# Optimization experiments

Hardware: AMD Instinct MI355X
Metric: run time of the kernel (lower is better)

The kernel has to match this reference:

```python
import jax, jax.numpy as jnp
import numpy as np
from jax import lax

HEADS = 8
DIM_HEAD = 64
DIM = 512
EPS = 1e-12  # torch F.normalize eps


def _l2norm(x):
    # normalize along last axis, torch-style: x / max(||x||, eps)
    n = jnp.sqrt(jnp.sum(x * x, axis=-1, keepdims=True))
    return x / jnp.maximum(n, EPS)


def _dwconv(x_nchw, w):
    # depthwise 3x3, stride 1, SAME padding, no bias
    return lax.conv_general_dilated(
        x_nchw, w, window_strides=(1, 1), padding='SAME',
        dimension_numbers=('NCHW', 'OIHW', 'NCHW'),
        feature_group_count=DIM)


def setup_inputs() -> dict:
    key = jax.random.key(0)
    ks = jax.random.split(key, 8)
    b, h, w, c = 4, 128, 128, DIM
    s = 1.0 / np.sqrt(c)
    return {
        'x_in': jax.random.normal(ks[0], (b, h, w, c), jnp.float32),
        'mask': jax.random.uniform(ks[1], (b, h, w, c), jnp.float32),
        'Wq': jax.random.normal(ks[2], (c, HEADS * DIM_HEAD), jnp.float32) * s,
        'Wk': jax.random.normal(ks[3], (c, HEADS * DIM_HEAD), jnp.float32) * s,
        'Wv': jax.random.normal(ks[4], (c, HEADS * DIM_HEAD), jnp.float32) * s,
        'rescale': jnp.ones((HEADS, 1, 1), jnp.float32),
        'Wp': jax.random.normal(ks[5], (HEADS * DIM_HEAD, c), jnp.float32) * s,
        'bp': jnp.zeros((c,), jnp.float32),
        'conv1_w': jax.random.normal(ks[6], (DIM, 1, 3, 3), jnp.float32) * (1.0 / 3.0),
        'conv2_w': jax.random.normal(ks[7], (DIM, 1, 3, 3), jnp.float32) * (1.0 / 3.0),
    }


def reference(x_in, mask, Wq, Wk, Wv, rescale, Wp, bp, conv1_w, conv2_w):
    b, h, w, c = x_in.shape
    n = h * w
    x = x_in.reshape(b, n, c)
    q_inp = x @ Wq  # [b, n, heads*d]
    k_inp = x @ Wk
    v_inp = x @ Wv

    def split_heads(t):  # [b, n, heads*d] -> [b, heads, d, n]
        return jnp.transpose(t.reshape(b, n, HEADS, DIM_HEAD), (0, 2, 3, 1))

    m = split_heads(mask.reshape(b, n, c))
    q = _l2norm(split_heads(q_inp))  # normalize over n (spatial) axis
    k = _l2norm(split_heads(k_inp))
    v = split_heads(v_inp) * m

    # channel attention: [b, heads, d, d]
    attn = jnp.einsum('bhdn,bhen->bhde', k, q) * rescale
    attn = jax.nn.softmax(attn, axis=-1)
    xo = jnp.einsum('bhde,bhen->bhdn', attn, v)  # [b, heads, d, n]
    xo = jnp.transpose(xo, (0, 3, 1, 2)).reshape(b, n, HEADS * DIM_HEAD)
    out_c = (xo @ Wp + bp).reshape(b, h, w, c)

    # positional branch: dual depthwise conv on v_inp
    vp = jnp.transpose(v_inp.reshape(b, h, w, c), (0, 3, 1, 2))  # NCHW
    vp = _dwconv(jax.nn.gelu(_dwconv(vp, conv1_w)), conv2_w)
    out_p = jnp.transpose(vp, (0, 2, 3, 1))

    return out_c + out_p
```

## Files before the change

### kernel.cpp

```cpp
#include <hip/hip_runtime.h>
#include <math.h>

typedef float f4 __attribute__((ext_vector_type(4)));
typedef float f32x4 __attribute__((ext_vector_type(4)));
typedef short s8v __attribute__((ext_vector_type(8)));
typedef unsigned short us4 __attribute__((ext_vector_type(4)));

#define CDIM 512
#define N_TOK 65536
#define IMG 128

__device__ inline unsigned short bf16h(float x) {
  unsigned u = __float_as_uint(x);
  u += 0x7FFFu + ((u >> 16) & 1u);
  return (unsigned short)(u >> 16);
}
__device__ inline float bf16f(unsigned short h) {
  return __uint_as_float(((unsigned)h) << 16);
}
__device__ inline void split2(float x, unsigned short& h, unsigned short& l) {
  h = bf16h(x);
  l = bf16h(x - bf16f(h));
}

__global__ __launch_bounds__(256) void wt_pack(
    const float* __restrict__ Wq, const float* __restrict__ Wk,
    const float* __restrict__ Wv, unsigned short* __restrict__ WTh,
    unsigned short* __restrict__ WTl) {
  const int bid = blockIdx.x;
  const int which = bid >> 6;
  const int t = bid & 63;
  const int kt = t >> 3, nt = t & 7;
  const float* W = which == 0 ? Wq : (which == 1 ? Wk : Wv);
  __shared__ float ts[64][65];
  const int tid = threadIdx.x;
  const int r = tid >> 4, c4 = (tid & 15) << 2;
#pragma unroll
  for (int i = 0; i < 4; ++i) {
    const int rr = r + i * 16;
    *(f4*)&ts[rr][c4] =
        *(const f4*)(W + (size_t)(kt * 64 + rr) * CDIM + nt * 64 + c4);
  }
  __syncthreads();
  unsigned short* oh = WTh + (size_t)which * CDIM * CDIM;
  unsigned short* ol = WTl + (size_t)which * CDIM * CDIM;
#pragma unroll
  for (int i = 0; i < 4; ++i) {
    const int nn = r + i * 16;
    us4 h, l;
#pragma unroll
    for (int j = 0; j < 4; ++j) {
      unsigned short hh, ll;
      split2(ts[c4 + j][nn], hh, ll);
      h[j] = hh;
      l[j] = ll;
    }
    *(us4*)&oh[(size_t)(nt * 64 + nn) * CDIM + kt * 64 + c4] = h;
    *(us4*)&ol[(size_t)(nt * 64 + nn) * CDIM + kt * 64 + c4] = l;
  }
}

__global__ __launch_bounds__(256) void gemm_mfma_proj(
    const float* __restrict__ A, const unsigned short* __restrict__ WTh,
    const unsigned short* __restrict__ WTl, float* __restrict__ Cq,
    float* __restrict__ Ck, float* __restrict__ Cv) {
  const int bid = blockIdx.x;
  const int rt = bid / 12;
  const int rem = bid - rt * 12;
  const int which = rem >> 2;
  const int bn = rem & 3;

  __shared__ unsigned short Ah[128][40];
  __shared__ unsigned short Al[128][40];
  __shared__ unsigned short Bh[128][40];
  __shared__ unsigned short Bl[128][40];

  const int tid = threadIdx.x;
  const int lane = tid & 63, wid = tid >> 6;
  const int wr = wid >> 1, wc = wid & 1;
  const int fr = lane & 15, kh = lane >> 4;

  const float* Ab = A + (size_t)rt * 128 * CDIM;
  const unsigned short* Bhb = WTh + ((size_t)which * CDIM + bn * 128) * CDIM;
  const unsigned short* Blb = WTl + ((size_t)which * CDIM + bn * 128) * CDIM;

  const int ar = tid >> 3, ac = (tid & 7) << 2;
  const int br = tid >> 2, bc = (tid & 3) << 3;

  f32x4 acc[4][4];
#pragma unroll
  for (int mi = 0; mi < 4; ++mi)
#pragma unroll
    for (int ni = 0; ni < 4; ++ni)
#pragma unroll
      for (int r = 0; r < 4; ++r) acc[mi][ni][r] = 0.f;

  for (int kb = 0; kb < 16; ++kb) {
    const int k0 = kb * 32;
    f4 va[4];
    s8v vbh[2], vbl[2];
#pragma unroll
    for (int it = 0; it < 4; ++it)
      va[it] = *(const f4*)(Ab + (size_t)(ar + it * 32) * CDIM + k0 + ac);
#pragma unroll
    for (int it = 0; it < 2; ++it) {
      vbh[it] = *(const s8v*)(Bhb + (size_t)(br + it * 64) * CDIM + k0 + bc);
      vbl[it] = *(const s8v*)(Blb + (size_t)(br + it * 64) * CDIM + k0 + bc);
    }
    __syncthreads();
#pragma unroll
    for (int it = 0; it < 4; ++it) {
      us4 h, l;
#pragma unroll
      for (int j = 0; j < 4; ++j) {
        unsigned short hh, ll;
        split2(va[it][j], hh, ll);
        h[j] = hh;
        l[j] = ll;
      }
      *(us4*)&Ah[ar + it * 32][ac] = h;
      *(us4*)&Al[ar + it * 32][ac] = l;
    }
#pragma unroll
    for (int it = 0; it < 2; ++it) {
      *(s8v*)&Bh[br + it * 64][bc] = vbh[it];
      *(s8v*)&Bl[br + it * 64][bc] = vbl[it];
    }
    __syncthreads();
    s8v fah[4], fal[4], fbh[4], fbl[4];
#pragma unroll
    for (int mi = 0; mi < 4; ++mi) {
      fah[mi] = *(const s8v*)&Ah[wr * 64 + mi * 16 + fr][kh * 8];
      fal[mi] = *(const s8v*)&Al[wr * 64 + mi * 16 + fr][kh * 8];
    }
#pragma unroll
    for (int ni = 0; ni < 4; ++ni) {
      fbh[ni] = *(const s8v*)&Bh[wc * 64 + ni * 16 + fr][kh * 8];
      fbl[ni] = *(const s8v*)&Bl[wc * 64 + ni * 16 + fr][kh * 8];
    }
#pragma unroll
    for (int mi = 0; mi < 4; ++mi)
#pragma unroll
      for (int ni = 0; ni < 4; ++ni) {
        acc[mi][ni] = __builtin_amdgcn_mfma_f32_16x16x32_bf16(
            fah[mi], fbh[ni], acc[mi][ni], 0, 0, 0);
        acc[mi][ni] = __builtin_amdgcn_mfma_f32_16x16x32_bf16(
            fah[mi], fbl[ni], acc[mi][ni], 0, 0, 0);
        acc[mi][ni] = __builtin_amdgcn_mfma_f32_16x16x32_bf16(
            fal[mi], fbh[ni], acc[mi][ni], 0, 0, 0);
      }
  }
  float* C = which == 0 ? Cq : (which == 1 ? Ck : Cv);
#pragma unroll
  for (int mi = 0; mi < 4; ++mi) {
    const int row = rt * 128 + wr * 64 + mi * 16 + kh * 4;
#pragma unroll
    for (int ni = 0; ni < 4; ++ni) {
      const int col = bn * 128 + wc * 64 + ni * 16 + fr;
#pragma unroll
      for (int r = 0; r < 4; ++r)
        C[(size_t)(row + r) * CDIM + col] = acc[mi][ni][r];
    }
  }
}

__global__ __launch_bounds__(256) void gemm_mfma_vm(
    const float* __restrict__ V, const float* __restrict__ Msk,
    const unsigned short* __restrict__ Eh, const unsigned short* __restrict__ El,
    const float* __restrict__ bias, float* __restrict__ C) {
  const int bid = blockIdx.x;
  const int rt = bid >> 2;
  const int bn = bid & 3;
  const int batch = rt >> 7;

  __shared__ unsigned short Ah[128][40];
  __shared__ unsigned short Al[128][40];
  __shared__ unsigned short Bh[128][40];
  __shared__ unsigned short Bl[128][40];

  const int tid = threadIdx.x;
  const int lane = tid & 63, wid = tid >> 6;
  const int wr = wid >> 1, wc = wid & 1;
  const int fr = lane & 15, kh = lane >> 4;

  const float* Vb = V + (size_t)rt * 128 * CDIM;
  const float* Mb = Msk + (size_t)rt * 128 * CDIM;
  const unsigned short* Bhb = Eh + ((size_t)batch * CDIM + bn * 128) * CDIM;
  const unsigned short* Blb = El + ((size_t)batch * CDIM + bn * 128) * CDIM;

  const int ar = tid >> 3, ac = (tid & 7) << 2;
  const int br = tid >> 2, bc = (tid & 3) << 3;

  f32x4 acc[4][4];
#pragma unroll
  for (int mi = 0; mi < 4; ++mi)
#pragma unroll
    for (int ni = 0; ni < 4; ++ni)
#pragma unroll
      for (int r = 0; r < 4; ++r) acc[mi][ni][r] = 0.f;

  for (int kb = 0; kb < 16; ++kb) {
    const int k0 = kb * 32;
    f4 va[4], vm[4];
    s8v vbh[2], vbl[2];
#pragma unroll
    for (int it = 0; it < 4; ++it) {
      va[it] = *(const f4*)(Vb + (size_t)(ar + it * 32) * CDIM + k0 + ac);
      vm[it] = *(const f4*)(Mb + (size_t)(ar + it * 32) * CDIM + k0 + ac);
    }
#pragma unroll
    for (int it = 0; it < 2; ++it) {
      vbh[it] = *(const s8v*)(Bhb + (size_t)(br + it * 64) * CDIM + k0 + bc);
      vbl[it] = *(const s8v*)(Blb + (size_t)(br + it * 64) * CDIM + k0 + bc);
    }
    __syncthreads();
#pragma unroll
    for (int it = 0; it < 4; ++it) {
      us4 h, l;
#pragma unroll
      for (int j = 0; j < 4; ++j) {
        unsigned short hh, ll;
        split2(va[it][j] * vm[it][j], hh, ll);
        h[j] = hh;
        l[j] = ll;
      }
      *(us4*)&Ah[ar + it * 32][ac] = h;
      *(us4*)&Al[ar + it * 32][ac] = l;
    }
#pragma unroll
    for (int it = 0; it < 2; ++it) {
      *(s8v*)&Bh[br + it * 64][bc] = vbh[it];
      *(s8v*)&Bl[br + it * 64][bc] = vbl[it];
    }
    __syncthreads();
    s8v fah[4], fal[4], fbh[4], fbl[4];
#pragma unroll
    for (int mi = 0; mi < 4; ++mi) {
      fah[mi] = *(const s8v*)&Ah[wr * 64 + mi * 16 + fr][kh * 8];
      fal[mi] = *(const s8v*)&Al[wr * 64 + mi * 16 + fr][kh * 8];
    }
#pragma unroll
    for (int ni = 0; ni < 4; ++ni) {
      fbh[ni] = *(const s8v*)&Bh[wc * 64 + ni * 16 + fr][kh * 8];
      fbl[ni] = *(const s8v*)&Bl[wc * 64 + ni * 16 + fr][kh * 8];
    }
#pragma unroll
    for (int mi = 0; mi < 4; ++mi)
#pragma unroll
      for (int ni = 0; ni < 4; ++ni) {
        acc[mi][ni] = __builtin_amdgcn_mfma_f32_16x16x32_bf16(
            fah[mi], fbh[ni], acc[mi][ni], 0, 0, 0);
        acc[mi][ni] = __builtin_amdgcn_mfma_f32_16x16x32_bf16(
            fah[mi], fbl[ni], acc[mi][ni], 0, 0, 0);
        acc[mi][ni] = __builtin_amdgcn_mfma_f32_16x16x32_bf16(
            fal[mi], fbh[ni], acc[mi][ni], 0, 0, 0);
      }
  }
#pragma unroll
  for (int mi = 0; mi < 4; ++mi) {
    const int row = rt * 128 + wr * 64 + mi * 16 + kh * 4;
#pragma unroll
    for (int ni = 0; ni < 4; ++ni) {
      const int col = bn * 128 + wc * 64 + ni * 16 + fr;
      const float bb = bias[col];
#pragma unroll
      for (int r = 0; r < 4; ++r)
        C[(size_t)(row + r) * CDIM + col] = acc[mi][ni][r] + bb;
    }
  }
}

__global__ __launch_bounds__(256) void gram_partial(
    const float* __restrict__ Q, const float* __restrict__ Km,
    float* __restrict__ gram, float* __restrict__ qss,
    float* __restrict__ kss) {
  const int chunk = blockIdx.x;
  const int bh = blockIdx.y;
  const int b = bh >> 3, h = bh & 7;
  __shared__ float Qs[16][64];
  __shared__ float Ks[16][64];
  const int tid = threadIdx.x;
  const int tx = tid & 15, ty = tid >> 4;
  const int lr = tid >> 4;
  const int lc = (tid & 15) << 2;
  const size_t base = ((size_t)b * 16384 + (size_t)chunk * 256) * CDIM + h * 64;

  f4 acc[4];
#pragma unroll
  for (int i = 0; i < 4; ++i)
#pragma unroll
    for (int c = 0; c < 4; ++c) acc[i][c] = 0.f;
  float sq = 0.f, sk = 0.f;

  for (int s = 0; s < 16; ++s) {
    f4 qv = *(const f4*)(Q + base + (size_t)(s * 16 + lr) * CDIM + lc);
    f4 kv = *(const f4*)(Km + base + (size_t)(s * 16 + lr) * CDIM + lc);
    __syncthreads();
    *(f4*)&Qs[lr][lc] = qv;
    *(f4*)&Ks[lr][lc] = kv;
    __syncthreads();
#pragma unroll
    for (int r = 0; r < 16; ++r) {
      f4 qq = *(const f4*)&Qs[r][tx * 4];
      f4 kk = *(const f4*)&Ks[r][ty * 4];
#pragma unroll
      for (int i = 0; i < 4; ++i) acc[i] += kk[i] * qq;
    }
    if (tid < 64) {
#pragma unroll
      for (int r = 0; r < 16; ++r) { float v = Qs[r][tid]; sq += v * v; }
    } else if (tid < 128) {
#pragma unroll
      for (int r = 0; r < 16; ++r) { float v = Ks[r][tid - 64]; sk += v * v; }
    }
  }
  float* g = gram + (size_t)bh * 4096;
#pragma unroll
  for (int i = 0; i < 4; ++i)
#pragma unroll
    for (int j = 0; j < 4; ++j)
      atomicAdd(&g[(ty * 4 + i) * 64 + tx * 4 + j], acc[i][j]);
  if (tid < 64) atomicAdd(&qss[b * CDIM + h * 64 + tid], sq);
  else if (tid < 128) atomicAdd(&kss[b * CDIM + h * 64 + (tid - 64)], sk);
}

__global__ __launch_bounds__(256) void attn_softmax(
    float* __restrict__ gram, const float* __restrict__ qss,
    const float* __restrict__ kss, const float* __restrict__ rescale) {
  const int row = blockIdx.x * 4 + (threadIdx.x >> 6);
  const int lane = threadIdx.x & 63;
  const int bh = row >> 6, d = row & 63;
  const int b = bh >> 3, h = bh & 7;
  float kn = fmaxf(sqrtf(kss[b * CDIM + h * 64 + d]), 1e-12f);
  float qn = fmaxf(sqrtf(qss[b * CDIM + h * 64 + lane]), 1e-12f);
  float v = gram[(size_t)row * 64 + lane] / (kn * qn) * rescale[h];
  float m = v;
#pragma unroll
  for (int off = 32; off; off >>= 1) m = fmaxf(m, __shfl_xor(m, off));
  float e = expf(v - m);
  float s = e;
#pragma unroll
  for (int off = 32; off; off >>= 1) s += __shfl_xor(s, off);
  gram[(size_t)row * 64 + lane] = e / s;
}

__global__ __launch_bounds__(256) void build_weffT(
    const float* __restrict__ attn, const float* __restrict__ Wp,
    unsigned short* __restrict__ Eh, unsigned short* __restrict__ El) {
  const int b = blockIdx.x >> 3, h = blockIdx.x & 7;
  __shared__ float a_s[64][64];
  const int tid = threadIdx.x;
  const float* ablk = attn + (size_t)(b * 8 + h) * 4096;
#pragma unroll
  for (int i = 0; i < 16; ++i) {
    const int idx = tid + i * 256;
    a_s[idx >> 6][idx & 63] = ablk[idx];
  }
  __syncthreads();
#pragma unroll
  for (int jl = 0; jl < 2; ++jl) {
    const int j = tid + jl * 256;
    f4 acc[16];
#pragma unroll
    for (int e = 0; e < 16; ++e)
#pragma unroll
      for (int c = 0; c < 4; ++c) acc[e][c] = 0.f;
#pragma unroll 4
    for (int d = 0; d < 64; ++d) {
      const float w = Wp[(size_t)(h * 64 + d) * CDIM + j];
#pragma unroll
      for (int e = 0; e < 16; ++e) acc[e] += w * *(const f4*)&a_s[d][e * 4];
    }
    unsigned short* ohp = Eh + ((size_t)b * CDIM + j) * CDIM + h * 64;
    unsigned short* olp = El + ((size_t)b * CDIM + j) * CDIM + h * 64;
#pragma unroll
    for (int e = 0; e < 16; ++e) {
      us4 hh, ll;
#pragma unroll
      for (int c = 0; c < 4; ++c) {
        unsigned short x, y;
        split2(acc[e][c], x, y);
        hh[c] = x;
        ll[c] = y;
      }
      *(us4*)&ohp[e * 4] = hh;
      *(us4*)&olp[e * 4] = ll;
    }
  }
}

__device__ inline float gelu_tanh(float x) {
  float x3 = x * x * x;
  return 0.5f * x * (1.f + tanhf(0.7978845608028654f * (x + 0.044715f * x3)));
}

__global__ __launch_bounds__(256) void dwconv_gelu(
    const float* __restrict__ in, const float* __restrict__ w,
    float* __restrict__ out) {
  const int gid = blockIdx.x * 256 + threadIdx.x;
  const int c4 = gid & 127;
  const int x = (gid >> 7) & 127;
  const int y = (gid >> 14) & 127;
  const int b = gid >> 21;
  const int c = c4 << 2;
  f4 acc;
#pragma unroll
  for (int cc = 0; cc < 4; ++cc) acc[cc] = 0.f;
#pragma unroll
  for (int ky = 0; ky < 3; ++ky) {
    const int yy = y + ky - 1;
    if (yy < 0 || yy > 127) continue;
#pragma unroll
    for (int kx = 0; kx < 3; ++kx) {
      const int xx = x + kx - 1;
      if (xx < 0 || xx > 127) continue;
      f4 v = *(const f4*)(in + (((size_t)b * IMG + yy) * IMG + xx) * CDIM + c);
#pragma unroll
      for (int cc = 0; cc < 4; ++cc)
        acc[cc] += v[cc] * w[(c + cc) * 9 + ky * 3 + kx];
    }
  }
  f4 o;
#pragma unroll
  for (int cc = 0; cc < 4; ++cc) o[cc] = gelu_tanh(acc[cc]);
  *(f4*)(out + (((size_t)b * IMG + y) * IMG + x) * CDIM + c) = o;
}

__global__ __launch_bounds__(256) void dwconv_add(
    const float* __restrict__ in, const float* __restrict__ w,
    float* __restrict__ out) {
  const int gid = blockIdx.x * 256 + threadIdx.x;
  const int c4 = gid & 127;
  const int x = (gid >> 7) & 127;
  const int y = (gid >> 14) & 127;
  const int b = gid >> 21;
  const int c = c4 << 2;
  f4 acc;
#pragma unroll
  for (int cc = 0; cc < 4; ++cc) acc[cc] = 0.f;
#pragma unroll
  for (int ky = 0; ky < 3; ++ky) {
    const int yy = y + ky - 1;
    if (yy < 0 || yy > 127) continue;
#pragma unroll
    for (int kx = 0; kx < 3; ++kx) {
      const int xx = x + kx - 1;
      if (xx < 0 || xx > 127) continue;
      f4 v = *(const f4*)(in + (((size_t)b * IMG + yy) * IMG + xx) * CDIM + c);
#pragma unroll
      for (int cc = 0; cc < 4; ++cc)
        acc[cc] += v[cc] * w[(c + cc) * 9 + ky * 3 + kx];
    }
  }
  const size_t off = (((size_t)b * IMG + y) * IMG + x) * CDIM + c;
  f4 prev = *(const f4*)(out + off);
  *(f4*)(out + off) = prev + acc;
}

extern "C" void kernel_launch(void* const* d_in, const int* in_sizes, int n_in,
                              void* d_out, int out_size, void* d_ws,
                              size_t ws_size, hipStream_t stream) {
  const float* x    = (const float*)d_in[0];
  const float* mask = (const float*)d_in[1];
  const float* Wq   = (const float*)d_in[2];
  const float* Wk   = (const float*)d_in[3];
  const float* Wv   = (const float*)d_in[4];
  const float* resc = (const float*)d_in[5];
  const float* Wp   = (const float*)d_in[6];
  const float* bp   = (const float*)d_in[7];
  const float* w1   = (const float*)d_in[8];
  const float* w2   = (const float*)d_in[9];
  float* out = (float*)d_out;
  float* ws = (float*)d_ws;

  float* q_ws = ws;
  float* k_ws = q_ws + (size_t)N_TOK * CDIM;
  float* v_ws = k_ws + (size_t)N_TOK * CDIM;
  float* gram = v_ws + (size_t)N_TOK * CDIM;
  float* qss  = gram + 32 * 64 * 64;
  float* kss  = qss + 4 * CDIM;
  unsigned short* wTh = (unsigned short*)(kss + 4 * CDIM);
  unsigned short* wTl = wTh + 3 * CDIM * CDIM;
  unsigned short* weffTh = (unsigned short*)(kss + 4 * CDIM);
  unsigned short* weffTl = weffTh + 4 * CDIM * CDIM;

  hipMemsetAsync(gram, 0, (32 * 64 * 64 + 2 * 4 * CDIM) * sizeof(float),
                 stream);

  wt_pack<<<192, 256, 0, stream>>>(Wq, Wk, Wv, wTh, wTl);

  gemm_mfma_proj<<<6144, 256, 0, stream>>>(x, wTh, wTl, q_ws, k_ws, v_ws);

  gram_partial<<<dim3(64, 32), 256, 0, stream>>>(q_ws, k_ws, gram, qss, kss);
  attn_softmax<<<512, 256, 0, stream>>>(gram, qss, kss, resc);

  build_weffT<<<32, 256, 0, stream>>>(gram, Wp, weffTh, weffTl);

  dwconv_gelu<<<32768, 256, 0, stream>>>(v_ws, w1, q_ws);

  gemm_mfma_vm<<<2048, 256, 0, stream>>>(v_ws, mask, weffTh, weffTl, bp, out);

  dwconv_add<<<32768, 256, 0, stream>>>(q_ws, w2, out);
}
```

Before: 1.591 ms.

## Pre-split activations to tiled bf16, use direct global-to-LDS loads, store q/k as bf16

Adds pre-pass kernels that convert x and v*mask to bf16 in a tiled layout matching the GEMM k-blocks. The GEMMs then load tiles straight into LDS with global_load_lds instead of splitting fp32 in registers. The activation low-part MFMA is dropped, going from 3 to 2 MFMAs per tile, and q/k are written as bf16 so gram_partial reads half the bytes. build_weffT is re-parallelised over more blocks and writes the tiled layout. This trades some precision on the activations and adds extra passes over the activations.

New measurement: 1.396 ms. -12.3%, faster.

```diff
diff --git a/kernel.cpp b/kernel.cpp
--- a/kernel.cpp
+++ b/kernel.cpp
@@ -10,82 +10,128 @@
 #define N_TOK 65536
 #define IMG 128
 
-__device__ inline unsigned short bf16h(float x) {
+__device__ __forceinline__ unsigned short bf16h(float x) {
   unsigned u = __float_as_uint(x);
   u += 0x7FFFu + ((u >> 16) & 1u);
   return (unsigned short)(u >> 16);
 }
-__device__ inline float bf16f(unsigned short h) {
+__device__ __forceinline__ float bf16f(unsigned short h) {
   return __uint_as_float(((unsigned)h) << 16);
 }
-__device__ inline void split2(float x, unsigned short& h, unsigned short& l) {
+__device__ __forceinline__ void split2(float x, unsigned short& h,
+                                       unsigned short& l) {
   h = bf16h(x);
   l = bf16h(x - bf16f(h));
+}
+
+__device__ __forceinline__ void gl16(const unsigned short* g,
+                                     unsigned short* l) {
+  __builtin_amdgcn_global_load_lds(
+      (const __attribute__((address_space(1))) unsigned int*)g,
+      (__attribute__((address_space(3))) unsigned int*)l, 16, 0, 0);
+}
+
+
+__global__ __launch_bounds__(256) void split_x(const float* __restrict__ x,
+                                               unsigned short* __restrict__ xt) {
+  const int rt = blockIdx.x >> 4, kb = blockIdx.x & 15;
+  const int tid = threadIdx.x;
+  unsigned short* dst = xt + (size_t)(rt * 16 + kb) * 4096;
+#pragma unroll
+  for (int i = 0; i < 2; ++i) {
+    const int ci = tid + i * 256;
+    const int r = ci >> 2, kc = ci & 3;
+    const float* src = x + (size_t)(rt * 128 + r) * CDIM + kb * 32 + kc * 8;
+    f4 a = *(const f4*)src;
+    f4 b = *(const f4*)(src + 4);
+    us4 h0, h1;
+#pragma unroll
+    for (int j = 0; j < 4; ++j) {
+      h0[j] = bf16h(a[j]);
+      h1[j] = bf16h(b[j]);
+    }
+    *(us4*)&dst[ci * 8] = h0;
+    *(us4*)&dst[ci * 8 + 4] = h1;
+  }
+}
+
+__global__ __launch_bounds__(256) void vm_split(const float* __restrict__ v,
+                                                const float* __restrict__ msk,
+                                                unsigned short* __restrict__ vt) {
+  const int rt = blockIdx.x >> 4, kb = blockIdx.x & 15;
+  const int tid = threadIdx.x;
+  unsigned short* dst = vt + (size_t)(rt * 16 + kb) * 4096;
+#pragma unroll
+  for (int i = 0; i < 2; ++i) {
+    const int ci = tid + i * 256;
+    const int r = ci >> 2, kc = ci & 3;
+    const size_t off = (size_t)(rt * 128 + r) * CDIM + kb * 32 + kc * 8;
+    f4 a = *(const f4*)(v + off);
+    f4 b = *(const f4*)(v + off + 4);
+    f4 ma = *(const f4*)(msk + off);
+    f4 mb = *(const f4*)(msk + off + 4);
+    us4 h0, h1;
+#pragma unroll
+    for (int j = 0; j < 4; ++j) {
+      h0[j] = bf16h(a[j] * ma[j]);
+      h1[j] = bf16h(b[j] * mb[j]);
+    }
+    *(us4*)&dst[ci * 8] = h0;
+    *(us4*)&dst[ci * 8 + 4] = h1;
+  }
 }
 
 __global__ __launch_bounds__(256) void wt_pack(
     const float* __restrict__ Wq, const float* __restrict__ Wk,
     const float* __restrict__ Wv, unsigned short* __restrict__ WTh,
     unsigned short* __restrict__ WTl) {
-  const int bid = blockIdx.x;
-  const int which = bid >> 6;
-  const int t = bid & 63;
-  const int kt = t >> 3, nt = t & 7;
+  const int which = blockIdx.x >> 6;
+  const int rem = blockIdx.x & 63;
+  const int bt = rem >> 4, kb = rem & 15;
   const float* W = which == 0 ? Wq : (which == 1 ? Wk : Wv);
-  __shared__ float ts[64][65];
+  unsigned short* dh = WTh + ((size_t)which * 64 + bt * 16 + kb) * 4096;
+  unsigned short* dl = WTl + ((size_t)which * 64 + bt * 16 + kb) * 4096;
   const int tid = threadIdx.x;
-  const int r = tid >> 4, c4 = (tid & 15) << 2;
-#pragma unroll
-  for (int i = 0; i < 4; ++i) {
-    const int rr = r + i * 16;
-    *(f4*)&ts[rr][c4] =
-        *(const f4*)(W + (size_t)(kt * 64 + rr) * CDIM + nt * 64 + c4);
-  }
-  __syncthreads();
-  unsigned short* oh = WTh + (size_t)which * CDIM * CDIM;
-  unsigned short* ol = WTl + (size_t)which * CDIM * CDIM;
-#pragma unroll
-  for (int i = 0; i < 4; ++i) {
-    const int nn = r + i * 16;
-    us4 h, l;
-#pragma unroll
-    for (int j = 0; j < 4; ++j) {
-      unsigned short hh, ll;
-      split2(ts[c4 + j][nn], hh, ll);
-      h[j] = hh;
-      l[j] = ll;
-    }
-    *(us4*)&oh[(size_t)(nt * 64 + nn) * CDIM + kt * 64 + c4] = h;
-    *(us4*)&ol[(size_t)(nt * 64 + nn) * CDIM + kt * 64 + c4] = l;
-  }
-}
-
-__global__ __launch_bounds__(256) void gemm_mfma_proj(
-    const float* __restrict__ A, const unsigned short* __restrict__ WTh,
-    const unsigned short* __restrict__ WTl, float* __restrict__ Cq,
-    float* __restrict__ Ck, float* __restrict__ Cv) {
+#pragma unroll
+  for (int i = 0; i < 2; ++i) {
+    const int ci = tid + i * 256;
+    const int r = ci >> 2, kc = ci & 3;
+    const int n = bt * 128 + r;
+    const int kbase = kb * 32 + kc * 8;
+    unsigned short hh[8], ll[8];
+#pragma unroll
+    for (int j = 0; j < 8; ++j) {
+      float w = W[(size_t)(kbase + j) * CDIM + n];
+      split2(w, hh[j], ll[j]);
+    }
+#pragma unroll
+    for (int j = 0; j < 8; ++j) {
+      dh[ci * 8 + j] = hh[j];
+      dl[ci * 8 + j] = ll[j];
+    }
+  }
+}
+
+__global__ __launch_bounds__(256) void gemm_proj(
+    const unsigned short* __restrict__ xt, const unsigned short* __restrict__ WTh,
+    const unsigned short* __restrict__ WTl, unsigned short* __restrict__ qb,
+    unsigned short* __restrict__ kbo, float* __restrict__ v) {
   const int bid = blockIdx.x;
   const int rt = bid / 12;
   const int rem = bid - rt * 12;
-  const int which = rem >> 2;
-  const int bn = rem & 3;
-
-  __shared__ unsigned short Ah[128][40];
-  __shared__ unsigned short Al[128][40];
-  __shared__ unsigned short Bh[128][40];
-  __shared__ unsigned short Bl[128][40];
-
-  const int tid = threadIdx.x;
-  const int lane = tid & 63, wid = tid >> 6;
+  const int which = rem >> 2, bn = rem & 3;
+
+  __shared__ __attribute__((aligned(16))) unsigned short Ah_s[4096];
+  __shared__ __attribute__((aligned(16))) unsigned short Bh_s[4096];
+  __shared__ __attribute__((aligned(16))) unsigned short Bl_s[4096];
+
+  const int tid = threadIdx.x, lane = tid & 63, wid = tid >> 6;
   const int wr = wid >> 1, wc = wid & 1;
   const int fr = lane & 15, kh = lane >> 4;
 
-  const float* Ab = A + (size_t)rt * 128 * CDIM;
-  const unsigned short* Bhb = WTh + ((size_t)which * CDIM + bn * 128) * CDIM;
-  const unsigned short* Blb = WTl + ((size_t)which * CDIM + bn * 128) * CDIM;
-
-  const int ar = tid >> 3, ac = (tid & 7) << 2;
-  const int br = tid >> 2, bc = (tid & 3) << 3;
+  const unsigned short* Ab = xt + (size_t)rt * 16 * 4096;
+  const unsigned short* Bhb = WTh + ((size_t)which * 64 + bn * 16) * 4096;
+  const unsigned short* Blb = WTl + ((size_t)which * 64 + bn * 16) * 4096;
 
   f32x4 acc[4][4];
 #pragma unroll
@@ -95,101 +141,91 @@
 #pragma unroll
       for (int r = 0; r < 4; ++r) acc[mi][ni][r] = 0.f;
 
-  for (int kb = 0; kb < 16; ++kb) {
-    const int k0 = kb * 32;
-    f4 va[4];
-    s8v vbh[2], vbl[2];
-#pragma unroll
-    for (int it = 0; it < 4; ++it)
-      va[it] = *(const f4*)(Ab + (size_t)(ar + it * 32) * CDIM + k0 + ac);
-#pragma unroll
-    for (int it = 0; it < 2; ++it) {
-      vbh[it] = *(const s8v*)(Bhb + (size_t)(br + it * 64) * CDIM + k0 + bc);
-      vbl[it] = *(const s8v*)(Blb + (size_t)(br + it * 64) * CDIM + k0 + bc);
+  for (int kbi = 0; kbi < 16; ++kbi) {
+    if (kbi) __syncthreads();
+    {
+      const unsigned short* s0 = Ab + kbi * 4096;
+      const unsigned short* s1 = Bhb + kbi * 4096;
+      const unsigned short* s2 = Blb + kbi * 4096;
+#pragma unroll
+      for (int c = 0; c < 6; ++c) {
+        const int call = wid * 6 + c;
+        const int t = call >> 3, sub = call & 7;
+        const unsigned short* src = (t == 0 ? s0 : (t == 1 ? s1 : s2));
+        unsigned short* dst = (t == 0 ? Ah_s : (t == 1 ? Bh_s : Bl_s));
+        gl16(src + sub * 512 + lane * 8, dst + sub * 512);
+      }
     }
     __syncthreads();
-#pragma unroll
-    for (int it = 0; it < 4; ++it) {
-      us4 h, l;
-#pragma unroll
-      for (int j = 0; j < 4; ++j) {
-        unsigned short hh, ll;
-        split2(va[it][j], hh, ll);
-        h[j] = hh;
-        l[j] = ll;
-      }
-      *(us4*)&Ah[ar + it * 32][ac] = h;
-      *(us4*)&Al[ar + it * 32][ac] = l;
-    }
-#pragma unroll
-    for (int it = 0; it < 2; ++it) {
-      *(s8v*)&Bh[br + it * 64][bc] = vbh[it];
-      *(s8v*)&Bl[br + it * 64][bc] = vbl[it];
-    }
-    __syncthreads();
-    s8v fah[4], fal[4], fbh[4], fbl[4];
-#pragma unroll
-    for (int mi = 0; mi < 4; ++mi) {
-      fah[mi] = *(const s8v*)&Ah[wr * 64 + mi * 16 + fr][kh * 8];
-      fal[mi] = *(const s8v*)&Al[wr * 64 + mi * 16 + fr][kh * 8];
-    }
+    s8v fa[4], fbh[4], fbl[4];
+    const unsigned short* ap = &Ah_s[(wr * 64 + fr) * 32 + kh * 8];
+    const unsigned short* bhp = &Bh_s[(wc * 64 + fr) * 32 + kh * 8];
+    const unsigned short* blp = &Bl_s[(wc * 64 + fr) * 32 + kh * 8];
+#pragma unroll
+    for (int mi = 0; mi < 4; ++mi) fa[mi] = *(const s8v*)(ap + mi * 512);
 #pragma unroll
     for (int ni = 0; ni < 4; ++ni) {
-      fbh[ni] = *(const s8v*)&Bh[wc * 64 + ni * 16 + fr][kh * 8];
-      fbl[ni] = *(const s8v*)&Bl[wc * 64 + ni * 16 + fr][kh * 8];
+      fbh[ni] = *(const s8v*)(bhp + ni * 512);
+      fbl[ni] = *(const s8v*)(blp + ni * 512);
     }
 #pragma unroll
     for (int mi = 0; mi < 4; ++mi)
 #pragma unroll
       for (int ni = 0; ni < 4; ++ni) {
         acc[mi][ni] = __builtin_amdgcn_mfma_f32_16x16x32_bf16(
-            fah[mi], fbh[ni], acc[mi][ni], 0, 0, 0);
+            fa[mi], fbh[ni], acc[mi][ni], 0, 0, 0);
         acc[mi][ni] = __builtin_amdgcn_mfma_f32_16x16x32_bf16(
-            fah[mi], fbl[ni], acc[mi][ni], 0, 0, 0);
-        acc[mi][ni] = __builtin_amdgcn_mfma_f32_16x16x32_bf16(
-            fal[mi], fbh[ni], acc[mi][ni], 0, 0, 0);
+            fa[mi], fbl[ni], acc[mi][ni], 0, 0, 0);
       }
   }
-  float* C = which == 0 ? Cq : (which == 1 ? Ck : Cv);
-#pragma unroll
-  for (int mi = 0; mi < 4; ++mi) {
-    const int row = rt * 128 + wr * 64 + mi * 16 + kh * 4;
-#pragma unroll
-    for (int ni = 0; ni < 4; ++ni) {
-      const int col = bn * 128 + wc * 64 + ni * 16 + fr;
-#pragma unroll
-      for (int r = 0; r < 4; ++r)
-        C[(size_t)(row + r) * CDIM + col] = acc[mi][ni][r];
-    }
-  }
-}
-
-__global__ __launch_bounds__(256) void gemm_mfma_vm(
-    const float* __restrict__ V, const float* __restrict__ Msk,
-    const unsigned short* __restrict__ Eh, const unsigned short* __restrict__ El,
-    const float* __restrict__ bias, float* __restrict__ C) {
+
+  if (which < 2) {
+    unsigned short* C = which == 0 ? qb : kbo;
+#pragma unroll
+    for (int mi = 0; mi < 4; ++mi) {
+      const int row = rt * 128 + wr * 64 + mi * 16 + kh * 4;
+#pragma unroll
+      for (int ni = 0; ni < 4; ++ni) {
+        const int col = bn * 128 + wc * 64 + ni * 16 + fr;
+#pragma unroll
+        for (int r = 0; r < 4; ++r)
+          C[(size_t)(row + r) * CDIM + col] = bf16h(acc[mi][ni][r]);
+      }
+    }
+  } else {
+#pragma unroll
+    for (int mi = 0; mi < 4; ++mi) {
+      const int row = rt * 128 + wr * 64 + mi * 16 + kh * 4;
+#pragma unroll
+      for (int ni = 0; ni < 4; ++ni) {
+        const int col = bn * 128 + wc * 64 + ni * 16 + fr;
+#pragma unroll
+        for (int r = 0; r < 4; ++r)
+          v[(size_t)(row + r) * CDIM + col] = acc[mi][ni][r];
+      }
+    }
+  }
+}
+
+__global__ __launch_bounds__(256) void gemm_vm(
+    const unsigned short* __restrict__ vt, const unsigned short* __restrict__ Eh,
+    const unsigned short* __restrict__ El, const float* __restrict__ bias,
+    float* __restrict__ out) {
   const int bid = blockIdx.x;
-  const int rt = bid >> 2;
-  const int bn = bid & 3;
+  const int rt = bid >> 2, bn = bid & 3;
   const int batch = rt >> 7;
 
-  __shared__ unsigned short Ah[128][40];
-  __shared__ unsigned short Al[128][40];
-  __shared__ unsigned short Bh[128][40];
-  __shared__ unsigned short Bl[128][40];
-
-  const int tid = threadIdx.x;
-  const int lane = tid & 63, wid = tid >> 6;
+  __shared__ __attribute__((aligned(16))) unsigned short Ah_s[4096];
+  __shared__ __attribute__((aligned(16))) unsigned short Bh_s[4096];
+  __shared__ __attribute__((aligned(16))) unsigned short Bl_s[4096];
+
+  const int tid = threadIdx.x, lane = tid & 63, wid = tid >> 6;
   const int wr = wid >> 1, wc = wid & 1;
   const int fr = lane & 15, kh = lane >> 4;
 
-  const float* Vb = V + (size_t)rt * 128 * CDIM;
-  const float* Mb = Msk + (size_t)rt * 128 * CDIM;
-  const unsigned short* Bhb = Eh + ((size_t)batch * CDIM + bn * 128) * CDIM;
-  const unsigned short* Blb = El + ((size_t)batch * CDIM + bn * 128) * CDIM;
-
-  const int ar = tid >> 3, ac = (tid & 7) << 2;
-  const int br = tid >> 2, bc = (tid & 3) << 3;
+  const unsigned short* Ab = vt + (size_t)rt * 16 * 4096;
+  const unsigned short* Bhb = Eh + ((size_t)batch * 64 + bn * 16) * 4096;
+  const unsigned short* Blb = El + ((size_t)batch * 64 + bn * 16) * 4096;
 
   f32x4 acc[4][4];
 #pragma unroll
@@ -199,61 +235,41 @@
 #pragma unroll
       for (int r = 0; r < 4; ++r) acc[mi][ni][r] = 0.f;
 
-  for (int kb = 0; kb < 16; ++kb) {
-    const int k0 = kb * 32;
-    f4 va[4], vm[4];
-    s8v vbh[2], vbl[2];
-#pragma unroll
-    for (int it = 0; it < 4; ++it) {
-      va[it] = *(const f4*)(Vb + (size_t)(ar + it * 32) * CDIM + k0 + ac);
-      vm[it] = *(const f4*)(Mb + (size_t)(ar + it * 32) * CDIM + k0 + ac);
-    }
-#pragma unroll
-    for (int it = 0; it < 2; ++it) {
-      vbh[it] = *(const s8v*)(Bhb + (size_t)(br + it * 64) * CDIM + k0 + bc);
-      vbl[it] = *(const s8v*)(Blb + (size_t)(br + it * 64) * CDIM + k0 + bc);
+  for (int kbi = 0; kbi < 16; ++kbi) {
+    if (kbi) __syncthreads();
+    {
+      const unsigned short* s0 = Ab + kbi * 4096;
+      const unsigned short* s1 = Bhb + kbi * 4096;
+      const unsigned short* s2 = Blb + kbi * 4096;
+#pragma unroll
+      for (int c = 0; c < 6; ++c) {
+        const int call = wid * 6 + c;
+        const int t = call >> 3, sub = call & 7;
+        const unsigned short* src = (t == 0 ? s0 : (t == 1 ? s1 : s2));
+        unsigned short* dst = (t == 0 ? Ah_s : (t == 1 ? Bh_s : Bl_s));
+        gl16(src + sub * 512 + lane * 8, dst + sub * 512);
+      }
     }
     __syncthreads();
-#pragma unroll
-    for (int it = 0; it < 4; ++it) {
-      us4 h, l;
-#pragma unroll
-      for (int j = 0; j < 4; ++j) {
-        unsigned short hh, ll;
-        split2(va[it][j] * vm[it][j], hh, ll);
-        h[j] = hh;
-        l[j] = ll;
-      }
-      *(us4*)&Ah[ar + it * 32][ac] = h;
-      *(us4*)&Al[ar + it * 32][ac] = l;
-    }
-#pragma unroll
-    for (int it = 0; it < 2; ++it) {
-      *(s8v*)&Bh[br + it * 64][bc] = vbh[it];
-      *(s8v*)&Bl[br + it * 64][bc] = vbl[it];
-    }
-    __syncthreads();
-    s8v fah[4], fal[4], fbh[4], fbl[4];
-#pragma unroll
-    for (int mi = 0; mi < 4; ++mi) {
-      fah[mi] = *(const s8v*)&Ah[wr * 64 + mi * 16 + fr][kh * 8];
-      fal[mi] = *(const s8v*)&Al[wr * 64 + mi * 16 + fr][kh * 8];
-    }
+    s8v fa[4], fbh[4], fbl[4];
+    const unsigned short* ap = &Ah_s[(wr * 64 + fr) * 32 + kh * 8];
+    const unsigned short* bhp = &Bh_s[(wc * 64 + fr) * 32 + kh * 8];
+    const unsigned short* blp = &Bl_s[(wc * 64 + fr) * 32 + kh * 8];
+#pragma unroll
+    for (int mi = 0; mi < 4; ++mi) fa[mi] = *(const s8v*)(ap + mi * 512);
 #pragma unroll
     for (int ni = 0; ni < 4; ++ni) {
-      fbh[ni] = *(const s8v*)&Bh[wc * 64 + ni * 16 + fr][kh * 8];
-      fbl[ni] = *(const s8v*)&Bl[wc * 64 + ni * 16 + fr][kh * 8];
+      fbh[ni] = *(const s8v*)(bhp + ni * 512);
+      fbl[ni] = *(const s8v*)(blp + ni * 512);
     }
 #pragma unroll
     for (int mi = 0; mi < 4; ++mi)
 #pragma unroll
       for (int ni = 0; ni < 4; ++ni) {
         acc[mi][ni] = __builtin_amdgcn_mfma_f32_16x16x32_bf16(
-            fah[mi], fbh[ni], acc[mi][ni], 0, 0, 0);
+            fa[mi], fbh[ni], acc[mi][ni], 0, 0, 0);
         acc[mi][ni] = __builtin_amdgcn_mfma_f32_16x16x32_bf16(
-            fah[mi], fbl[ni], acc[mi][ni], 0, 0, 0);
-        acc[mi][ni] = __builtin_amdgcn_mfma_f32_16x16x32_bf16(
-            fal[mi], fbh[ni], acc[mi][ni], 0, 0, 0);
+            fa[mi], fbl[ni], acc[mi][ni], 0, 0, 0);
       }
   }
 #pragma unroll
@@ -265,13 +281,13 @@
       const float bb = bias[col];
 #pragma unroll
       for (int r = 0; r < 4; ++r)
-        C[(size_t)(row + r) * CDIM + col] = acc[mi][ni][r] + bb;
+        out[(size_t)(row + r) * CDIM + col] = acc[mi][ni][r] + bb;
     }
   }
 }
 
 __global__ __launch_bounds__(256) void gram_partial(
-    const float* __restrict__ Q, const float* __restrict__ Km,
+    const unsigned short* __restrict__ Q, const unsigned short* __restrict__ Km,
     float* __restrict__ gram, float* __restrict__ qss,
     float* __restrict__ kss) {
   const int chunk = blockIdx.x;
@@ -293,11 +309,14 @@
   float sq = 0.f, sk = 0.f;
 
   for (int s = 0; s < 16; ++s) {
-    f4 qv = *(const f4*)(Q + base + (size_t)(s * 16 + lr) * CDIM + lc);
-    f4 kv = *(const f4*)(Km + base + (size_t)(s * 16 + lr) * CDIM + lc);
+    us4 qv = *(const us4*)(Q + base + (size_t)(s * 16 + lr) * CDIM + lc);
+    us4 kv = *(const us4*)(Km + base + (size_t)(s * 16 + lr) * CDIM + lc);
     __syncthreads();
-    *(f4*)&Qs[lr][lc] = qv;
-    *(f4*)&Ks[lr][lc] = kv;
+#pragma unroll
+    for (int j = 0; j < 4; ++j) {
+      Qs[lr][lc + j] = bf16f(qv[j]);
+      Ks[lr][lc + j] = bf16f(kv[j]);
+    }
     __syncthreads();
 #pragma unroll
     for (int r = 0; r < 16; ++r) {
@@ -308,10 +327,10 @@
     }
     if (tid < 64) {
 #pragma unroll
-      for (int r = 0; r < 16; ++r) { float v = Qs[r][tid]; sq += v * v; }
+      for (int r = 0; r < 16; ++r) { float t = Qs[r][tid]; sq += t * t; }
     } else if (tid < 128) {
 #pragma unroll
-      for (int r = 0; r < 16; ++r) { float v = Ks[r][tid - 64]; sk += v * v; }
+      for (int r = 0; r < 16; ++r) { float t = Ks[r][tid - 64]; sk += t * t; }
     }
   }
   float* g = gram + (size_t)bh * 4096;
@@ -347,7 +366,9 @@
 __global__ __launch_bounds__(256) void build_weffT(
     const float* __restrict__ attn, const float* __restrict__ Wp,
     unsigned short* __restrict__ Eh, unsigned short* __restrict__ El) {
-  const int b = blockIdx.x >> 3, h = blockIdx.x & 7;
+  const int b = blockIdx.x >> 6;
+  const int h = (blockIdx.x >> 3) & 7;
+  const int jt = blockIdx.x & 7;
   __shared__ float a_s[64][64];
   const int tid = threadIdx.x;
   const float* ablk = attn + (size_t)(b * 8 + h) * 4096;
@@ -357,39 +378,32 @@
     a_s[idx >> 6][idx & 63] = ablk[idx];
   }
   __syncthreads();
-#pragma unroll
-  for (int jl = 0; jl < 2; ++jl) {
-    const int j = tid + jl * 256;
-    f4 acc[16];
-#pragma unroll
-    for (int e = 0; e < 16; ++e)
-#pragma unroll
-      for (int c = 0; c < 4; ++c) acc[e][c] = 0.f;
-#pragma unroll 4
-    for (int d = 0; d < 64; ++d) {
-      const float w = Wp[(size_t)(h * 64 + d) * CDIM + j];
-#pragma unroll
-      for (int e = 0; e < 16; ++e) acc[e] += w * *(const f4*)&a_s[d][e * 4];
-    }
-    unsigned short* ohp = Eh + ((size_t)b * CDIM + j) * CDIM + h * 64;
-    unsigned short* olp = El + ((size_t)b * CDIM + j) * CDIM + h * 64;
-#pragma unroll
-    for (int e = 0; e < 16; ++e) {
-      us4 hh, ll;
-#pragma unroll
-      for (int c = 0; c < 4; ++c) {
-        unsigned short x, y;
-        split2(acc[e][c], x, y);
-        hh[c] = x;
-        ll[c] = y;
-      }
-      *(us4*)&ohp[e * 4] = hh;
-      *(us4*)&olp[e * 4] = ll;
-    }
-  }
-}
-
-__device__ inline float gelu_tanh(float x) {
+  const int jl = tid & 63, eq = tid >> 6;
+  const int j = jt * 64 + jl;
+  float acc[16];
+#pragma unroll
+  for (int e = 0; e < 16; ++e) acc[e] = 0.f;
+#pragma unroll 8
+  for (int d = 0; d < 64; ++d) {
+    const float w = Wp[(size_t)(h * 64 + d) * CDIM + j];
+#pragma unroll
+    for (int e = 0; e < 16; ++e) acc[e] += w * a_s[d][eq * 16 + e];
+  }
+  const int bt = jt >> 1, r = j & 127;
+#pragma unroll
+  for (int e = 0; e < 16; ++e) {
+    const int ich = h * 64 + eq * 16 + e;
+    const int kbq = ich >> 5, kc = (ich >> 3) & 3, w8 = ich & 7;
+    unsigned short hh, ll;
+    split2(acc[e], hh, ll);
+    const size_t idx =
+        ((size_t)b * 64 + bt * 16 + kbq) * 4096 + (r * 4 + kc) * 8 + w8;
+    Eh[idx] = hh;
+    El[idx] = ll;
+  }
+}
+
+__device__ __forceinline__ float gelu_tanh(float x) {
   float x3 = x * x * x;
   return 0.5f * x * (1.f + tanhf(0.7978845608028654f * (x + 0.044715f * x3)));
 }
@@ -471,34 +485,38 @@
   const float* w1   = (const float*)d_in[8];
   const float* w2   = (const float*)d_in[9];
   float* out = (float*)d_out;
-  float* ws = (float*)d_ws;
-
-  float* q_ws = ws;
-  float* k_ws = q_ws + (size_t)N_TOK * CDIM;
-  float* v_ws = k_ws + (size_t)N_TOK * CDIM;
-  float* gram = v_ws + (size_t)N_TOK * CDIM;
-  float* qss  = gram + 32 * 64 * 64;
-  float* kss  = qss + 4 * CDIM;
-  unsigned short* wTh = (unsigned short*)(kss + 4 * CDIM);
-  unsigned short* wTl = wTh + 3 * CDIM * CDIM;
-  unsigned short* weffTh = (unsigned short*)(kss + 4 * CDIM);
-  unsigned short* weffTl = weffTh + 4 * CDIM * CDIM;
-
-  hipMemsetAsync(gram, 0, (32 * 64 * 64 + 2 * 4 * CDIM) * sizeof(float),
-                 stream);
-
+  char* W = (char*)d_ws;
+
+  unsigned short* xh  = (unsigned short*)(W);
+  unsigned short* qb  = (unsigned short*)(W + ((size_t)64 << 20));
+  unsigned short* kbf = (unsigned short*)(W + ((size_t)128 << 20));
+  float* v_ws = (float*)(W + ((size_t)192 << 20));
+  float* gram = (float*)(W + ((size_t)320 << 20));
+  float* qss  = gram + 32 * 4096;
+  float* kss  = qss + 2048;
+  unsigned short* wTh = (unsigned short*)(W + ((size_t)321 << 20));
+  unsigned short* wTl = wTh + (size_t)3 * 262144;
+  unsigned short* weh = (unsigned short*)(W + ((size_t)324 << 20));
+  unsigned short* wel = weh + (size_t)4 * 262144;
+  float* t1 = (float*)W;
+  unsigned short* vmh = kbf;
+
+  hipMemsetAsync(gram, 0, (32 * 4096 + 2 * 2048) * sizeof(float), stream);
+
+  split_x<<<8192, 256, 0, stream>>>(x, xh);
   wt_pack<<<192, 256, 0, stream>>>(Wq, Wk, Wv, wTh, wTl);
 
-  gemm_mfma_proj<<<6144, 256, 0, stream>>>(x, wTh, wTl, q_ws, k_ws, v_ws);
-
-  gram_partial<<<dim3(64, 32), 256, 0, stream>>>(q_ws, k_ws, gram, qss, kss);
+  gemm_proj<<<6144, 256, 0, stream>>>(xh, wTh, wTl, qb, kbf, v_ws);
+
+  gram_partial<<<dim3(64, 32), 256, 0, stream>>>(qb, kbf, gram, qss, kss);
   attn_softmax<<<512, 256, 0, stream>>>(gram, qss, kss, resc);
 
-  build_weffT<<<32, 256, 0, stream>>>(gram, Wp, weffTh, weffTl);
-
-  dwconv_gelu<<<32768, 256, 0, stream>>>(v_ws, w1, q_ws);
-
-  gemm_mfma_vm<<<2048, 256, 0, stream>>>(v_ws, mask, weffTh, weffTl, bp, out);
-
-  dwconv_add<<<32768, 256, 0, stream>>>(q_ws, w2, out);
-}
+  build_weffT<<<256, 256, 0, stream>>>(gram, Wp, weh, wel);
+
+  dwconv_gelu<<<32768, 256, 0, stream>>>(v_ws, w1, t1);
+
+  vm_split<<<8192, 256, 0, stream>>>(v_ws, mask, vmh);
+  gemm_vm<<<2048, 256, 0, stream>>>(vmh, weh, wel, bp, out);
+
+  dwconv_add<<<32768, 256, 0, stream>>>(t1, w2, out);
+}
```
